# Performance work log

Hardware: AMD Instinct MI355X
Metric: run time of the kernel (lower is better)

## Reference

```python
import jax, jax.numpy as jnp
import numpy as np

B, DIN, HID, COMP = 16384, 1024, 512, 64

def setup_inputs() -> dict:
    key = jax.random.key(0)
    ks = jax.random.split(key, 16)
    s = lambda fan_in: 1.0 / np.sqrt(fan_in)
    return {
        "x1": jax.random.normal(ks[0], (B, DIN), jnp.float32),
        "x2": jax.random.normal(ks[1], (B, DIN), jnp.float32),
        "Wb1": jax.random.normal(ks[2], (DIN, HID), jnp.float32) * s(DIN),
        "bb1": jnp.zeros((HID,), jnp.float32),
        "Wb2": jax.random.normal(ks[3], (DIN, HID), jnp.float32) * s(DIN),
        "bb2": jnp.zeros((HID,), jnp.float32),
        "Wc1": jax.random.normal(ks[4], (HID, COMP), jnp.float32) * s(HID),
        "bc1": jnp.zeros((COMP,), jnp.float32),
        "Wc2": jax.random.normal(ks[5], (HID, COMP), jnp.float32) * s(HID),
        "bc2": jnp.zeros((COMP,), jnp.float32),
        "Wf1": jax.random.normal(ks[6], (COMP * COMP, 64), jnp.float32) * s(COMP * COMP),
        "bf1": jnp.zeros((64,), jnp.float32),
        "Wf2": jax.random.normal(ks[7], (64, 2), jnp.float32) * s(64),
        "bf2": jnp.zeros((2,), jnp.float32),
    }

def reference(x1, x2, Wb1, bb1, Wb2, bb2, Wc1, bc1, Wc2, bc2, Wf1, bf1, Wf2, bf2):
    # branch + compress: [B, DIN] -> [B, HID] -> [B, COMP]
    f1 = (jax.nn.relu(x1 @ Wb1 + bb1)) @ Wc1 + bc1  # [B, 64]
    f2 = (jax.nn.relu(x2 @ Wb2 + bb2)) @ Wc2 + bc2  # [B, 64]
    # kronecker_product(f1, f2): per-sample (f2 col) * (f1 row) -> [64,64], row-major flatten
    # element at flat index p*64 + q is f2[p] * f1[q]
    kron = jnp.einsum('bp,bq->bpq', f2, f1).reshape(f1.shape[0], -1)  # [B, 4096]
    h = kron @ Wf1 + bf1   # [B, 64]
    out = h @ Wf2 + bf2    # [B, 2]
    return out
```

## Files before the change

### kernel.cpp

```cpp
#include <hip/hip_runtime.h>

#define B_SZ 16384
#define DIN  1024
#define HID  512
#define COMP 64

typedef __bf16 bf16_t;
typedef __bf16 bf16x4 __attribute__((ext_vector_type(4)));
typedef __bf16 bf16x8 __attribute__((ext_vector_type(8)));
typedef float  f32x4  __attribute__((ext_vector_type(4)));

__device__ __forceinline__ void gl2lds16(const void* g, void* l) {
    __builtin_amdgcn_global_load_lds(
        (const __attribute__((address_space(1))) void*)g,
        (__attribute__((address_space(3))) void*)l, 16, 0, 0);
}

__global__ __launch_bounds__(256) void k_prep(
    const float* __restrict__ Wb1, const float* __restrict__ Wb2,
    bf16_t* __restrict__ wbt1, bf16_t* __restrict__ wbt2,
    const float* __restrict__ Wc1, const float* __restrict__ Wc2,
    bf16_t* __restrict__ wct1, bf16_t* __restrict__ wct2,
    const float* __restrict__ Wf1, const float* __restrict__ bf1v,
    const float* __restrict__ Wf2, const float* __restrict__ bf2v,
    const float* __restrict__ bc1, const float* __restrict__ bc2,
    float* __restrict__ f1, float* __restrict__ f2,
    const float* __restrict__ x1, const float* __restrict__ x2,
    bf16_t* __restrict__ xb1, bf16_t* __restrict__ xb2,
    float* __restrict__ G, float* __restrict__ c)
{
    const int bid = blockIdx.x, tid = threadIdx.x;

    if (bid >= 3152) {
        const int l = bid - 3152;
        const int z = l >> 13;
        const float* x  = z ? x2  : x1;
        bf16_t*      xb = z ? xb2 : xb1;
        const size_t base = ((size_t)(l & 8191) * 256 + tid) * 8;
        float4 v0 = *reinterpret_cast<const float4*>(x + base);
        float4 v1 = *reinterpret_cast<const float4*>(x + base + 4);
        bf16x8 o;
        o[0] = (bf16_t)v0.x; o[1] = (bf16_t)v0.y;
        o[2] = (bf16_t)v0.z; o[3] = (bf16_t)v0.w;
        o[4] = (bf16_t)v1.x; o[5] = (bf16_t)v1.y;
        o[6] = (bf16_t)v1.z; o[7] = (bf16_t)v1.w;
        *reinterpret_cast<bf16x8*>(xb + base) = o;
        return;
    }

    __shared__ float tile[32][33];
    const int tx = tid & 31, ty = tid >> 5;

    if (bid < 1024) {
        const int z = bid >> 9, t = bid & 511;
        const float* in  = z ? Wb2  : Wb1;
        bf16_t*      out = z ? wbt2 : wbt1;
        const int n0 = (t & 15) * 32, k0 = (t >> 4) * 32;
        #pragma unroll
        for (int i = 0; i < 4; i++)
            tile[ty + i * 8][tx] = in[(size_t)(k0 + ty + i * 8) * HID + n0 + tx];
        __syncthreads();
        #pragma unroll
        for (int i = 0; i < 4; i++)
            out[(size_t)(n0 + ty + i * 8) * DIN + k0 + tx] = (bf16_t)tile[tx][ty + i * 8];
    } else if (bid < 1088) {
        const int l = bid - 1024;
        const int z = l >> 5, t = l & 31;
        const float* in  = z ? Wc2  : Wc1;
        bf16_t*      out = z ? wct2 : wct1;
        const int n0 = (t & 1) * 32, k0 = (t >> 1) * 32;
        #pragma unroll
        for (int i = 0; i < 4; i++)
            tile[ty + i * 8][tx] = in[(size_t)(k0 + ty + i * 8) * COMP + n0 + tx];
        __syncthreads();
        #pragma unroll
        for (int i = 0; i < 4; i++)
            out[(size_t)(n0 + ty + i * 8) * HID + k0 + tx] = (bf16_t)tile[tx][ty + i * 8];
    } else if (bid < 1104) {
        const int i = (bid - 1088) * 256 + tid;
        float a0 = 0.f, a1 = 0.f;
        #pragma unroll 8
        for (int o = 0; o < 64; o++) {
            float w = Wf1[(size_t)i * 64 + o];
            a0 = fmaf(w, Wf2[o * 2 + 0], a0);
            a1 = fmaf(w, Wf2[o * 2 + 1], a1);
        }
        G[i]        = a0;
        G[4096 + i] = a1;
        if (i < 2) {
            float s = bf2v[i];
            for (int o = 0; o < 64; o++) s = fmaf(bf1v[o], Wf2[o * 2 + i], s);
            c[i] = s;
        }
    } else {
        const int l = bid - 1104;
        const int z = l >> 10;
        const float* bc = z ? bc2 : bc1;
        float*       f  = z ? f2  : f1;
        const int i = (l & 1023) * 256 + tid;
        const int c4 = (i & 15) * 4;
        float4 v = make_float4(bc[c4], bc[c4 + 1], bc[c4 + 2], bc[c4 + 3]);
        reinterpret_cast<float4*>(f)[i] = v;
    }
}

__global__ __launch_bounds__(256) void k_gemm1f(
    const bf16_t* __restrict__ XB1, const bf16_t* __restrict__ XB2,
    const bf16_t* __restrict__ WT1, const bf16_t* __restrict__ WT2,
    const float* __restrict__ bias1, const float* __restrict__ bias2,
    const bf16_t* __restrict__ WC1, const bf16_t* __restrict__ WC2,
    float* __restrict__ F1, float* __restrict__ F2)
{
    const int bid = blockIdx.x;
    const int xcd = bid & 7, s = bid >> 3;
    const int nb = s & 3;
    const int G  = (s >> 2) * 8 + xcd;
    const int mb = G >> 1, z = G & 1;

    const bf16_t* XB   = z ? XB2   : XB1;
    const bf16_t* WT   = z ? WT2   : WT1;
    const float*  bias = z ? bias2 : bias1;
    const bf16_t* WC   = z ? WC2   : WC1;
    float*        F    = z ? F2    : F1;

    const int m0 = mb * 128;
    const int n0 = nb * 128;

    __shared__ char smem[33792];
    bf16_t* As[2] = { (bf16_t*)smem,           (bf16_t*)(smem + 8192)  };
    bf16_t* Bs[2] = { (bf16_t*)(smem + 16384), (bf16_t*)(smem + 24576) };
    bf16_t* Hs    = (bf16_t*)smem;

    const int tid  = threadIdx.x;
    const int lane = tid & 63;
    const int wave = tid >> 6;
    const int wr   = (wave >> 1) * 64;
    const int wc   = (wave & 1) * 64;
    const int l15  = lane & 15;
    const int g4   = lane >> 4;
    const int lk   = g4 * 8;

    f32x4 acc[4][4] = {};

    for (int k0 = 0; k0 < DIN; k0 += 64) {
        #pragma unroll
        for (int u = 0; u < 2; u++) {
            #pragma unroll
            for (int i = 0; i < 2; i++) {
                int cc = i * 256 + tid;
                int r = cc >> 2, kh = (cc & 3) * 8;
                gl2lds16(&XB[(size_t)(m0 + r) * DIN + k0 + u * 32 + kh], &As[u][cc * 8]);
                gl2lds16(&WT[(size_t)(n0 + r) * DIN + k0 + u * 32 + kh], &Bs[u][cc * 8]);
            }
        }
        __syncthreads();

        #pragma unroll
        for (int u = 0; u < 2; u++) {
            bf16x8 af[4], bfv[4];
            #pragma unroll
            for (int mi = 0; mi < 4; mi++)
                af[mi] = *reinterpret_cast<const bf16x8*>(
                    &As[u][(wr + mi * 16 + l15) * 32 + lk]);
            #pragma unroll
            for (int ni = 0; ni < 4; ni++)
                bfv[ni] = *reinterpret_cast<const bf16x8*>(
                    &Bs[u][(wc + ni * 16 + l15) * 32 + lk]);
            #pragma unroll
            for (int mi = 0; mi < 4; mi++)
                #pragma unroll
                for (int ni = 0; ni < 4; ni++)
                    acc[mi][ni] = __builtin_amdgcn_mfma_f32_16x16x32_bf16(
                        af[mi], bfv[ni], acc[mi][ni], 0, 0, 0);
        }
        __syncthreads();
    }

    float bv[4];
    #pragma unroll
    for (int ni = 0; ni < 4; ni++)
        bv[ni] = bias[n0 + wc + ni * 16 + l15];
    #pragma unroll
    for (int mi = 0; mi < 4; mi++) {
        int lr = wr + mi * 16 + g4 * 4;
        #pragma unroll
        for (int ni = 0; ni < 4; ni++) {
            int colL = wc + ni * 16 + l15;
            #pragma unroll
            for (int r = 0; r < 4; r++) {
                float v = fmaxf(acc[mi][ni][r] + bv[ni], 0.0f);
                Hs[(lr + r) * 132 + colL] = (bf16_t)v;
            }
        }
    }
    __syncthreads();

    f32x4 acc2[2][4] = {};
    #pragma unroll
    for (int kk = 0; kk < 128; kk += 32) {
        bf16x8 af[2];
        #pragma unroll
        for (int m2 = 0; m2 < 2; m2++)
            af[m2] = *reinterpret_cast<const bf16x8*>(
                &Hs[(wave * 32 + m2 * 16 + l15) * 132 + kk + lk]);
        #pragma unroll
        for (int ni = 0; ni < 4; ni++) {
            bf16x8 bw = *reinterpret_cast<const bf16x8*>(
                &WC[(size_t)(ni * 16 + l15) * HID + n0 + kk + lk]);
            #pragma unroll
            for (int m2 = 0; m2 < 2; m2++)
                acc2[m2][ni] = __builtin_amdgcn_mfma_f32_16x16x32_bf16(
                    af[m2], bw, acc2[m2][ni], 0, 0, 0);
        }
    }
    #pragma unroll
    for (int m2 = 0; m2 < 2; m2++) {
        int rbase = m0 + wave * 32 + m2 * 16 + g4 * 4;
        #pragma unroll
        for (int ni = 0; ni < 4; ni++) {
            int col = ni * 16 + l15;
            #pragma unroll
            for (int r = 0; r < 4; r++)
                unsafeAtomicAdd(&F[(size_t)(rbase + r) * COMP + col], acc2[m2][ni][r]);
        }
    }
}

__global__ __launch_bounds__(256) void k_bilinear(
    const float* __restrict__ f1, const float* __restrict__ f2,
    const float* __restrict__ G, const float* __restrict__ c,
    float* __restrict__ out)
{
    __shared__ float Gs[2][4096];
    const int tid = threadIdx.x;
    for (int i = tid; i < 2048; i += 256)
        reinterpret_cast<float4*>(&Gs[0][0])[i] =
            reinterpret_cast<const float4*>(G)[i];
    const float c0 = c[0], c1 = c[1];
    __syncthreads();

    const int lane = tid & 63;
    const int wave = tid >> 6;
    const int base = (blockIdx.x * 4 + wave) * 4;

    for (int s = 0; s < 4; s++) {
        const int b = base + s;
        const float f1q = f1[(size_t)b * 64 + lane];
        const float f2q = f2[(size_t)b * 64 + lane];
        float a0 = 0.f, a1 = 0.f;
        #pragma unroll 8
        for (int p = 0; p < 64; p++) {
            float s2 = __shfl(f2q, p);
            a0 = fmaf(s2, Gs[0][p * 64 + lane], a0);
            a1 = fmaf(s2, Gs[1][p * 64 + lane], a1);
        }
        a0 *= f1q;
        a1 *= f1q;
        #pragma unroll
        for (int off = 32; off > 0; off >>= 1) {
            a0 += __shfl_xor(a0, off);
            a1 += __shfl_xor(a1, off);
        }
        if (lane == 0) {
            out[(size_t)b * 2 + 0] = a0 + c0;
            out[(size_t)b * 2 + 1] = a1 + c1;
        }
    }
}

extern "C" void kernel_launch(void* const* d_in, const int* in_sizes, int n_in,
                              void* d_out, int out_size, void* d_ws, size_t ws_size,
                              hipStream_t stream)
{
    const float* x1  = (const float*)d_in[0];
    const float* x2  = (const float*)d_in[1];
    const float* Wb1 = (const float*)d_in[2];
    const float* bb1 = (const float*)d_in[3];
    const float* Wb2 = (const float*)d_in[4];
    const float* bb2 = (const float*)d_in[5];
    const float* Wc1 = (const float*)d_in[6];
    const float* bc1 = (const float*)d_in[7];
    const float* Wc2 = (const float*)d_in[8];
    const float* bc2 = (const float*)d_in[9];
    const float* Wf1 = (const float*)d_in[10];
    const float* bf1v = (const float*)d_in[11];
    const float* Wf2 = (const float*)d_in[12];
    const float* bf2v = (const float*)d_in[13];
    float* out = (float*)d_out;

    char* ws = (char*)d_ws;
    bf16_t* wbt1 = (bf16_t*)ws; ws += (size_t)HID * DIN * 2;
    bf16_t* wbt2 = (bf16_t*)ws; ws += (size_t)HID * DIN * 2;
    bf16_t* wct1 = (bf16_t*)ws; ws += (size_t)COMP * HID * 2;
    bf16_t* wct2 = (bf16_t*)ws; ws += (size_t)COMP * HID * 2;
    bf16_t* xb1  = (bf16_t*)ws; ws += (size_t)B_SZ * DIN * 2;
    bf16_t* xb2  = (bf16_t*)ws; ws += (size_t)B_SZ * DIN * 2;
    float*  f1   = (float*)ws;  ws += (size_t)B_SZ * COMP * 4;
    float*  f2   = (float*)ws;  ws += (size_t)B_SZ * COMP * 4;
    float*  G    = (float*)ws;  ws += (size_t)2 * 4096 * 4;
    float*  c    = (float*)ws;  ws += 256;

    k_prep<<<19536, 256, 0, stream>>>(Wb1, Wb2, wbt1, wbt2,
                                      Wc1, Wc2, wct1, wct2,
                                      Wf1, bf1v, Wf2, bf2v,
                                      bc1, bc2, f1, f2,
                                      x1, x2, xb1, xb2, G, c);
    k_gemm1f<<<1024, 256, 0, stream>>>(xb1, xb2, wbt1, wbt2, bb1, bb2,
                                       wct1, wct2, f1, f2);
    k_bilinear<<<1024, 256, 0, stream>>>(f1, f2, G, c, out);
}
```

Before: 262.6 us.

## Rewrite branch GEMM with 256x256 tiles, swizzled LDS and interleaved prefetch

Tiles for the first GEMM grow from 128x128 to 256x256, with 512-thread blocks and 8 waves. The grid is 256 blocks and the block-to-tile mapping is XCD-aware. The LDS layout uses an XOR swizzle and is double-buffered, and the global-to-LDS prefetch for the next K step is split into quarters between MFMA phases. s_setprio is raised around the MFMA bursts. The aim is to raise arithmetic intensity per LDS byte, hide load latency, and do more of the compress GEMM per atomic. The cost is one block per CU with about 132KB of LDS, a single-wave grid with no tail balancing, and high register pressure from 32 accumulators.

```diff
diff --git a/kernel.cpp b/kernel.cpp
--- a/kernel.cpp
+++ b/kernel.cpp
@@ -9,6 +9,8 @@
 typedef __bf16 bf16x4 __attribute__((ext_vector_type(4)));
 typedef __bf16 bf16x8 __attribute__((ext_vector_type(8)));
 typedef float  f32x4  __attribute__((ext_vector_type(4)));
+
+#define MFMA16 __builtin_amdgcn_mfma_f32_16x16x32_bf16
 
 __device__ __forceinline__ void gl2lds16(const void* g, void* l) {
     __builtin_amdgcn_global_load_lds(
@@ -104,7 +106,7 @@
     }
 }
 
-__global__ __launch_bounds__(256) void k_gemm1f(
+__global__ __launch_bounds__(512, 2) void k_gemm1f(
     const bf16_t* __restrict__ XB1, const bf16_t* __restrict__ XB2,
     const bf16_t* __restrict__ WT1, const bf16_t* __restrict__ WT2,
     const float* __restrict__ bias1, const float* __restrict__ bias2,
@@ -112,10 +114,10 @@
     float* __restrict__ F1, float* __restrict__ F2)
 {
     const int bid = blockIdx.x;
-    const int xcd = bid & 7, s = bid >> 3;
-    const int nb = s & 3;
-    const int G  = (s >> 2) * 8 + xcd;
-    const int mb = G >> 1, z = G & 1;
+    const int nid = (bid & 7) * 32 + (bid >> 3);
+    const int z   = nid >> 7;
+    const int nb  = (nid >> 6) & 1;
+    const int mb  = nid & 63;
 
     const bf16_t* XB   = z ? XB2   : XB1;
     const bf16_t* WT   = z ? WT2   : WT1;
@@ -123,73 +125,164 @@
     const bf16_t* WC   = z ? WC2   : WC1;
     float*        F    = z ? F2    : F1;
 
-    const int m0 = mb * 128;
-    const int n0 = nb * 128;
-
-    __shared__ char smem[33792];
-    bf16_t* As[2] = { (bf16_t*)smem,           (bf16_t*)(smem + 8192)  };
-    bf16_t* Bs[2] = { (bf16_t*)(smem + 16384), (bf16_t*)(smem + 24576) };
-    bf16_t* Hs    = (bf16_t*)smem;
+    const int m0 = mb * 256;
+    const int n0 = nb * 256;
+
+    __shared__ __align__(128) char smem[135168];
 
     const int tid  = threadIdx.x;
     const int lane = tid & 63;
     const int wave = tid >> 6;
-    const int wr   = (wave >> 1) * 64;
-    const int wc   = (wave & 1) * 64;
+    const int wm   = wave >> 2;
+    const int wn   = wave & 3;
     const int l15  = lane & 15;
     const int g4   = lane >> 4;
-    const int lk   = g4 * 8;
-
-    f32x4 acc[4][4] = {};
-
-    for (int k0 = 0; k0 < DIN; k0 += 64) {
-        #pragma unroll
-        for (int u = 0; u < 2; u++) {
-            #pragma unroll
-            for (int i = 0; i < 2; i++) {
-                int cc = i * 256 + tid;
-                int r = cc >> 2, kh = (cc & 3) * 8;
-                gl2lds16(&XB[(size_t)(m0 + r) * DIN + k0 + u * 32 + kh], &As[u][cc * 8]);
-                gl2lds16(&WT[(size_t)(n0 + r) * DIN + k0 + u * 32 + kh], &Bs[u][cc * 8]);
+
+    const int srow = tid >> 3;
+    const int sch  = (tid & 7) ^ (srow & 7);
+    const bf16_t* gA = XB + (size_t)(m0 + srow) * DIN + sch * 8;
+    const bf16_t* gB = WT + (size_t)(n0 + srow) * DIN + sch * 8;
+    const int ldst = tid * 16;
+
+    const int l7   = l15 & 7;
+    const int lch0 = (g4 ^ l7) * 16;
+    const int lch1 = ((4 + g4) ^ l7) * 16;
+    const int arow = (wm * 128 + l15) * 128;
+    const int brow = (wn * 64  + l15) * 128;
+
+    f32x4 acc[8][4] = {};
+
+    #pragma unroll
+    for (int i = 0; i < 4; i++) {
+        gl2lds16(gA + (size_t)(i * 64) * DIN, smem + i * 8192 + ldst);
+        gl2lds16(gB + (size_t)(i * 64) * DIN, smem + 65536 + i * 8192 + ldst);
+    }
+    asm volatile("s_waitcnt vmcnt(0)" ::: "memory");
+    __builtin_amdgcn_s_barrier();
+    __builtin_amdgcn_sched_barrier(0);
+
+    bf16x8 a[4][2], b[4][2];
+
+    #pragma unroll 1
+    for (int kt = 0; kt < 16; ++kt) {
+        const int d = kt & 1;
+        const char* Ac = smem + d * 32768;
+        const char* Bc = smem + 65536 + d * 32768;
+        char* An = (char*)smem + (d ^ 1) * 32768;
+        char* Bn = (char*)smem + 65536 + (d ^ 1) * 32768;
+        const bf16_t* gAn = gA + (kt + 1) * 64;
+        const bf16_t* gBn = gB + (kt + 1) * 64;
+        const bool pf = (kt < 15);
+
+        #pragma unroll
+        for (int mi = 0; mi < 4; mi++) {
+            a[mi][0] = *(const bf16x8*)(Ac + arow + mi * 2048 + lch0);
+            a[mi][1] = *(const bf16x8*)(Ac + arow + mi * 2048 + lch1);
+        }
+        #pragma unroll
+        for (int ni = 0; ni < 2; ni++) {
+            b[ni][0] = *(const bf16x8*)(Bc + brow + ni * 2048 + lch0);
+            b[ni][1] = *(const bf16x8*)(Bc + brow + ni * 2048 + lch1);
+        }
+        if (pf) {
+            gl2lds16(gAn,                     An + ldst);
+            gl2lds16(gAn + (size_t)64 * DIN,  An + 8192 + ldst);
+        }
+        __builtin_amdgcn_s_barrier();
+        __builtin_amdgcn_sched_barrier(0);
+        __builtin_amdgcn_s_setprio(1);
+        #pragma unroll
+        for (int mi = 0; mi < 4; mi++)
+            #pragma unroll
+            for (int ni = 0; ni < 2; ni++) {
+                acc[mi][ni] = MFMA16(a[mi][0], b[ni][0], acc[mi][ni], 0, 0, 0);
+                acc[mi][ni] = MFMA16(a[mi][1], b[ni][1], acc[mi][ni], 0, 0, 0);
             }
-        }
-        __syncthreads();
-
-        #pragma unroll
-        for (int u = 0; u < 2; u++) {
-            bf16x8 af[4], bfv[4];
-            #pragma unroll
-            for (int mi = 0; mi < 4; mi++)
-                af[mi] = *reinterpret_cast<const bf16x8*>(
-                    &As[u][(wr + mi * 16 + l15) * 32 + lk]);
-            #pragma unroll
-            for (int ni = 0; ni < 4; ni++)
-                bfv[ni] = *reinterpret_cast<const bf16x8*>(
-                    &Bs[u][(wc + ni * 16 + l15) * 32 + lk]);
-            #pragma unroll
-            for (int mi = 0; mi < 4; mi++)
-                #pragma unroll
-                for (int ni = 0; ni < 4; ni++)
-                    acc[mi][ni] = __builtin_amdgcn_mfma_f32_16x16x32_bf16(
-                        af[mi], bfv[ni], acc[mi][ni], 0, 0, 0);
-        }
-        __syncthreads();
-    }
-
+        __builtin_amdgcn_s_setprio(0);
+        __builtin_amdgcn_s_barrier();
+        __builtin_amdgcn_sched_barrier(0);
+
+        #pragma unroll
+        for (int ni = 2; ni < 4; ni++) {
+            b[ni][0] = *(const bf16x8*)(Bc + brow + ni * 2048 + lch0);
+            b[ni][1] = *(const bf16x8*)(Bc + brow + ni * 2048 + lch1);
+        }
+        if (pf) {
+            gl2lds16(gAn + (size_t)128 * DIN, An + 16384 + ldst);
+            gl2lds16(gAn + (size_t)192 * DIN, An + 24576 + ldst);
+        }
+        __builtin_amdgcn_s_barrier();
+        __builtin_amdgcn_sched_barrier(0);
+        __builtin_amdgcn_s_setprio(1);
+        #pragma unroll
+        for (int mi = 0; mi < 4; mi++)
+            #pragma unroll
+            for (int ni = 2; ni < 4; ni++) {
+                acc[mi][ni] = MFMA16(a[mi][0], b[ni][0], acc[mi][ni], 0, 0, 0);
+                acc[mi][ni] = MFMA16(a[mi][1], b[ni][1], acc[mi][ni], 0, 0, 0);
+            }
+        __builtin_amdgcn_s_setprio(0);
+        __builtin_amdgcn_s_barrier();
+        __builtin_amdgcn_sched_barrier(0);
+
+        #pragma unroll
+        for (int mi = 0; mi < 4; mi++) {
+            a[mi][0] = *(const bf16x8*)(Ac + arow + 8192 + mi * 2048 + lch0);
+            a[mi][1] = *(const bf16x8*)(Ac + arow + 8192 + mi * 2048 + lch1);
+        }
+        if (pf) {
+            gl2lds16(gBn,                     Bn + ldst);
+            gl2lds16(gBn + (size_t)64 * DIN,  Bn + 8192 + ldst);
+        }
+        __builtin_amdgcn_s_barrier();
+        __builtin_amdgcn_sched_barrier(0);
+        __builtin_amdgcn_s_setprio(1);
+        #pragma unroll
+        for (int mi = 0; mi < 4; mi++)
+            #pragma unroll
+            for (int ni = 0; ni < 2; ni++) {
+                acc[4 + mi][ni] = MFMA16(a[mi][0], b[ni][0], acc[4 + mi][ni], 0, 0, 0);
+                acc[4 + mi][ni] = MFMA16(a[mi][1], b[ni][1], acc[4 + mi][ni], 0, 0, 0);
+            }
+        __builtin_amdgcn_s_setprio(0);
+        __builtin_amdgcn_s_barrier();
+        __builtin_amdgcn_sched_barrier(0);
+
+        if (pf) {
+            gl2lds16(gBn + (size_t)128 * DIN, Bn + 16384 + ldst);
+            gl2lds16(gBn + (size_t)192 * DIN, Bn + 24576 + ldst);
+        }
+        __builtin_amdgcn_s_barrier();
+        __builtin_amdgcn_sched_barrier(0);
+        __builtin_amdgcn_s_setprio(1);
+        #pragma unroll
+        for (int mi = 0; mi < 4; mi++)
+            #pragma unroll
+            for (int ni = 2; ni < 4; ni++) {
+                acc[4 + mi][ni] = MFMA16(a[mi][0], b[ni][0], acc[4 + mi][ni], 0, 0, 0);
+                acc[4 + mi][ni] = MFMA16(a[mi][1], b[ni][1], acc[4 + mi][ni], 0, 0, 0);
+            }
+        __builtin_amdgcn_s_setprio(0);
+        if (pf) asm volatile("s_waitcnt vmcnt(0)" ::: "memory");
+        __builtin_amdgcn_s_barrier();
+        __builtin_amdgcn_sched_barrier(0);
+    }
+
+    bf16_t* Hs = (bf16_t*)smem;
     float bv[4];
     #pragma unroll
     for (int ni = 0; ni < 4; ni++)
-        bv[ni] = bias[n0 + wc + ni * 16 + l15];
+        bv[ni] = bias[n0 + wn * 64 + ni * 16 + l15];
     #pragma unroll
-    for (int mi = 0; mi < 4; mi++) {
-        int lr = wr + mi * 16 + g4 * 4;
+    for (int mi = 0; mi < 8; mi++) {
+        const int lr = wm * 128 + mi * 16 + g4 * 4;
         #pragma unroll
         for (int ni = 0; ni < 4; ni++) {
-            int colL = wc + ni * 16 + l15;
+            const int colL = wn * 64 + ni * 16 + l15;
             #pragma unroll
             for (int r = 0; r < 4; r++) {
                 float v = fmaxf(acc[mi][ni][r] + bv[ni], 0.0f);
-                Hs[(lr + r) * 132 + colL] = (bf16_t)v;
+                Hs[(lr + r) * 264 + colL] = (bf16_t)v;
             }
         }
     }
@@ -197,28 +290,25 @@
 
     f32x4 acc2[2][4] = {};
     #pragma unroll
-    for (int kk = 0; kk < 128; kk += 32) {
-        bf16x8 af[2];
+    for (int kk = 0; kk < 256; kk += 32) {
+        bf16x8 af2[2];
         #pragma unroll
         for (int m2 = 0; m2 < 2; m2++)
-            af[m2] = *reinterpret_cast<const bf16x8*>(
-                &Hs[(wave * 32 + m2 * 16 + l15) * 132 + kk + lk]);
+            af2[m2] = *(const bf16x8*)(Hs + (wave * 32 + m2 * 16 + l15) * 264 + kk + g4 * 8);
         #pragma unroll
         for (int ni = 0; ni < 4; ni++) {
-            bf16x8 bw = *reinterpret_cast<const bf16x8*>(
-                &WC[(size_t)(ni * 16 + l15) * HID + n0 + kk + lk]);
+            bf16x8 bw = *(const bf16x8*)(&WC[(size_t)(ni * 16 + l15) * HID + n0 + kk + g4 * 8]);
             #pragma unroll
             for (int m2 = 0; m2 < 2; m2++)
-                acc2[m2][ni] = __builtin_amdgcn_mfma_f32_16x16x32_bf16(
-                    af[m2], bw, acc2[m2][ni], 0, 0, 0);
+                acc2[m2][ni] = MFMA16(af2[m2], bw, acc2[m2][ni], 0, 0, 0);
         }
     }
     #pragma unroll
     for (int m2 = 0; m2 < 2; m2++) {
-        int rbase = m0 + wave * 32 + m2 * 16 + g4 * 4;
+        const int rbase = m0 + wave * 32 + m2 * 16 + g4 * 4;
         #pragma unroll
         for (int ni = 0; ni < 4; ni++) {
-            int col = ni * 16 + l15;
+            const int col = ni * 16 + l15;
             #pragma unroll
             for (int r = 0; r < 4; r++)
                 unsafeAtomicAdd(&F[(size_t)(rbase + r) * COMP + col], acc2[m2][ni][r]);
@@ -305,7 +395,7 @@
                                       Wf1, bf1v, Wf2, bf2v,
                                       bc1, bc2, f1, f2,
                                       x1, x2, xb1, xb2, G, c);
-    k_gemm1f<<<1024, 256, 0, stream>>>(xb1, xb2, wbt1, wbt2, bb1, bb2,
-                                       wct1, wct2, f1, f2);
+    k_gemm1f<<<256, 512, 0, stream>>>(xb1, xb2, wbt1, wbt2, bb1, bb2,
+                                      wct1, wct2, f1, f2);
     k_bilinear<<<1024, 256, 0, stream>>>(f1, f2, G, c, out);
 }
```

Result: faster. 249.2 us (-5.1%).
